# Optimization experiments

Measured on AMD Instinct MI355X. Metric: run time of the kernel, lower is better.

The kernel has to match this reference:

```python
import jax, jax.numpy as jnp
import numpy as np

N = 300000   # total nodes
C = 32       # hidden states
M = 64       # discrete label alphabet
NGEN = 8     # number of generative models
G = 8192     # number of graphs


def setup_inputs() -> dict:
    key = jax.random.key(0)
    k1, k2, k3, k4 = jax.random.split(key, 4)
    B = jax.random.uniform(k1, (C, M, NGEN), minval=-5.0, maxval=5.0, dtype=jnp.float32)
    Pi = jax.random.uniform(k2, (C, NGEN), minval=-5.0, maxval=5.0, dtype=jnp.float32)
    x = jax.random.randint(k3, (N,), 0, M)
    batch = jnp.sort(jax.random.randint(k4, (N,), 0, G))
    return {"B": B, "Pi": Pi, "x": x, "batch": batch, "num_graphs": G}


def reference(B, Pi, x, batch, num_graphs):
    # softmax reparameterization: over M for B, over C for Pi (per generator)
    sm_B = jax.nn.softmax(B, axis=1)          # (C, M, n_gen)
    sm_Pi = jax.nn.softmax(Pi, axis=0)        # (C, n_gen)
    # gather per-node emission probs, then joint with prior -> (N, C, n_gen)
    numerator = sm_Pi[None, :, :] * jnp.transpose(sm_B[:, x, :], (1, 0, 2))
    posterior = numerator / numerator.sum(axis=1, keepdims=True)  # (N, C, n_gen)
    likelihood = (posterior * jnp.log(numerator)).sum(axis=1)     # (N, n_gen)
    # scatter-sum per graph
    likelihood = jax.ops.segment_sum(likelihood, batch, num_segments=num_graphs)  # (G, n_gen)
    h_vals = posterior.max(axis=1, keepdims=True)   # (N, 1, n_gen)
    h_idx = posterior.argmax(axis=1)                # (N, n_gen)
    return likelihood, h_vals, h_idx
```

## Files before the change

kernel.cpp:

```cpp
#include <hip/hip_runtime.h>

#define C_DIM 32
#define M_DIM 64
#define NG    8
#define TAB   (M_DIM * NG)
#define ST    9
#define SPB   1024
#define NPB   512

__global__ void __launch_bounds__(256)
cgmm_prep(const float* __restrict__ B, const float* __restrict__ Pi,
          const int* __restrict__ batch,
          float* __restrict__ tab, int* __restrict__ starts,
          int N, int G, int nsb) {
    const int tid = threadIdx.x;

    if ((int)blockIdx.x < nsb) {
        const int base = blockIdx.x * SPB;
        for (int i = tid; i < SPB; i += 256) {
            const int n = base + i;
            if (n >= N) break;
            const int bn = batch[n];
            if (n == 0) {
                for (int j = 0; j <= bn; ++j) starts[j] = 0;
            } else {
                const int bp = batch[n - 1];
                for (int j = bp + 1; j <= bn; ++j) starts[j] = n;
            }
            if (n == N - 1) {
                for (int j = bn + 1; j <= G; ++j) starts[j] = N;
            }
        }
        return;
    }

    __shared__ float Pis[C_DIM * NG];
    __shared__ float lsePi_s[NG];
    __shared__ float K_s[C_DIM * NG];

    Pis[tid] = Pi[tid];
    __syncthreads();

    if (tid < NG) {
        float mx = -1e30f;
        #pragma unroll
        for (int c = 0; c < C_DIM; ++c) mx = fmaxf(mx, Pis[c * NG + tid]);
        float s = 0.f;
        #pragma unroll
        for (int c = 0; c < C_DIM; ++c) s += expf(Pis[c * NG + tid] - mx);
        lsePi_s[tid] = logf(s) + mx;
    }
    __syncthreads();

    {
        const int g = tid & 7;
        const float* bp = B + (tid >> 3) * (M_DIM * NG) + g;
        float mx = -1e30f;
        #pragma unroll
        for (int m = 0; m < M_DIM; ++m) mx = fmaxf(mx, bp[m * NG]);
        float s = 0.f;
        #pragma unroll
        for (int m = 0; m < M_DIM; ++m) s += expf(bp[m * NG] - mx);
        K_s[tid] = Pis[tid] - (logf(s) + mx) - lsePi_s[g];
    }
    __syncthreads();

    {
        const int q = tid >> 3, g = tid & 7;
        #pragma unroll
        for (int h = 0; h < 2; ++h) {
            const int m = q + 32 * h;
            float L[C_DIM];
            float best = -1e30f; int bidx = 0;
            #pragma unroll
            for (int c = 0; c < C_DIM; ++c) {
                float v = B[c * (M_DIM * NG) + m * NG + g] + K_s[c * NG + g];
                L[c] = v;
                if (v > best) { best = v; bidx = c; }
            }
            float se = 0.f, la = 0.f;
            #pragma unroll
            for (int c = 0; c < C_DIM; ++c) {
                float e = expf(L[c] - best);
                se += e; la += e * L[c];
            }
            const int idx = m * NG + g;
            tab[idx]           = la / se;
            tab[TAB + idx]     = 1.f / se;
            tab[2 * TAB + idx] = (float)bidx;
        }
    }
}

__global__ void __launch_bounds__(256)
cgmm_write(const int* __restrict__ x, const int* __restrict__ starts,
           const float* __restrict__ tab,
           float* __restrict__ out_like, float* __restrict__ out_hv,
           float* __restrict__ out_hi, int N, int G, int nnb) {
    const int tid = threadIdx.x;

    if ((int)blockIdx.x < nnb) {
        __shared__ float hval_s[M_DIM * ST];
        __shared__ float hidx_s[M_DIM * ST];
        __shared__ int   xs_s[NPB];
        const int base = blockIdx.x * NPB;

        for (int i = tid; i < TAB; i += 256) {
            const int m = i >> 3, g = i & 7;
            hval_s[m * ST + g] = tab[TAB + i];
            hidx_s[m * ST + g] = tab[2 * TAB + i];
        }
        for (int i = tid; i < NPB; i += 256) {
            const int n = base + i;
            if (n < N) xs_s[i] = x[n];
        }
        __syncthreads();

        const int s = tid >> 3, g = tid & 7;
        #pragma unroll
        for (int k = 0; k < NPB / 32; ++k) {
            const int i = k * 32 + s;
            const int n = base + i;
            if (n >= N) break;
            const int xm = xs_s[i];
            out_hv[(size_t)n * NG + g] = hval_s[xm * ST + g];
            out_hi[(size_t)n * NG + g] = hidx_s[xm * ST + g];
        }
        return;
    }

    __shared__ float like_s[M_DIM * ST];
    for (int i = tid; i < TAB; i += 256)
        like_s[(i >> 3) * ST + (i & 7)] = tab[i];
    __syncthreads();

    const int j = ((int)blockIdx.x - nnb) * 4 + (tid >> 6);
    if (j >= G) return;
    const int start = starts[j];
    const int end   = starts[j + 1];

    const int slot = (tid >> 3) & 7;
    const int g    = tid & 7;

    float acc = 0.f;
    for (int n = start + slot; n < end; n += 8)
        acc += like_s[x[n] * ST + g];

    acc += __shfl_xor(acc, 8);
    acc += __shfl_xor(acc, 16);
    acc += __shfl_xor(acc, 32);
    if ((tid & 63) < NG) out_like[(size_t)j * NG + g] = acc;
}

extern "C" void kernel_launch(void* const* d_in, const int* in_sizes, int n_in,
                              void* d_out, int out_size, void* d_ws, size_t ws_size,
                              hipStream_t stream) {
    const float* B     = (const float*)d_in[0];
    const float* Pi    = (const float*)d_in[1];
    const int*   x     = (const int*)d_in[2];
    const int*   batch = (const int*)d_in[3];
    const int N = in_sizes[2];
    const int G = (out_size - 2 * N * NG) / NG;

    float* tab    = (float*)d_ws;
    int*   starts = (int*)((char*)d_ws + 8192);

    float* out_like = (float*)d_out;
    float* out_hv   = out_like + (size_t)G * NG;
    float* out_hi   = out_hv + (size_t)N * NG;

    const int nsb = (N + SPB - 1) / SPB;
    const int nnb = (N + NPB - 1) / NPB;
    const int nlb = (G + 3) / 4;

    cgmm_prep<<<nsb + 1, 256, 0, stream>>>(B, Pi, batch, tab, starts, N, G, nsb);
    cgmm_write<<<nnb + nlb, 256, 0, stream>>>(x, starts, tab, out_like,
                                              out_hv, out_hi, N, G, nnb);
}
```

Before: 21.78 us.

## Fuse per-node hv/hi writes into per-graph segment loop; stage B in LDS

Result: faster. 19.98 us (-8.2%).

```diff
diff --git a/kernel.cpp b/kernel.cpp
--- a/kernel.cpp
+++ b/kernel.cpp
@@ -5,10 +5,10 @@
 #define NG    8
 #define TAB   (M_DIM * NG)
 #define ST    9
-#define SPB   1024
-#define NPB   512
+#define BST   520
+#define SPB   2048
 
-__global__ void __launch_bounds__(256)
+__global__ void __launch_bounds__(512)
 cgmm_prep(const float* __restrict__ B, const float* __restrict__ Pi,
           const int* __restrict__ batch,
           float* __restrict__ tab, int* __restrict__ starts,
@@ -17,7 +17,7 @@
 
     if ((int)blockIdx.x < nsb) {
         const int base = blockIdx.x * SPB;
-        for (int i = tid; i < SPB; i += 256) {
+        for (int i = tid; i < SPB; i += 512) {
             const int n = base + i;
             if (n >= N) break;
             const int bn = batch[n];
@@ -34,11 +34,20 @@
         return;
     }
 
+    __shared__ float Bs[C_DIM * BST];
     __shared__ float Pis[C_DIM * NG];
     __shared__ float lsePi_s[NG];
     __shared__ float K_s[C_DIM * NG];
 
-    Pis[tid] = Pi[tid];
+    {
+        const float4* B4 = (const float4*)B;
+        float4* Bs4 = (float4*)Bs;
+        #pragma unroll
+        for (int i = tid; i < (C_DIM * M_DIM * NG) / 4; i += 512) {
+            Bs4[(i >> 7) * (BST / 4) + (i & 127)] = B4[i];
+        }
+        if (tid < C_DIM * NG / 4) ((float4*)Pis)[tid] = ((const float4*)Pi)[tid];
+    }
     __syncthreads();
 
     if (tid < NG) {
@@ -52,9 +61,9 @@
     }
     __syncthreads();
 
-    {
-        const int g = tid & 7;
-        const float* bp = B + (tid >> 3) * (M_DIM * NG) + g;
+    if (tid < C_DIM * NG) {
+        const int c = tid >> 3, g = tid & 7;
+        const float* bp = Bs + c * BST + g;
         float mx = -1e30f;
         #pragma unroll
         for (int m = 0; m < M_DIM; ++m) mx = fmaxf(mx, bp[m * NG]);
@@ -66,29 +75,24 @@
     __syncthreads();
 
     {
-        const int q = tid >> 3, g = tid & 7;
+        const int m = tid >> 3, g = tid & 7;
+        float L[C_DIM];
+        float best = -1e30f; int bidx = 0;
         #pragma unroll
-        for (int h = 0; h < 2; ++h) {
-            const int m = q + 32 * h;
-            float L[C_DIM];
-            float best = -1e30f; int bidx = 0;
-            #pragma unroll
-            for (int c = 0; c < C_DIM; ++c) {
-                float v = B[c * (M_DIM * NG) + m * NG + g] + K_s[c * NG + g];
-                L[c] = v;
-                if (v > best) { best = v; bidx = c; }
-            }
-            float se = 0.f, la = 0.f;
-            #pragma unroll
-            for (int c = 0; c < C_DIM; ++c) {
-                float e = expf(L[c] - best);
-                se += e; la += e * L[c];
-            }
-            const int idx = m * NG + g;
-            tab[idx]           = la / se;
-            tab[TAB + idx]     = 1.f / se;
-            tab[2 * TAB + idx] = (float)bidx;
+        for (int c = 0; c < C_DIM; ++c) {
+            float v = Bs[c * BST + m * NG + g] + K_s[c * NG + g];
+            L[c] = v;
+            if (v > best) { best = v; bidx = c; }
         }
+        float se = 0.f, la = 0.f;
+        #pragma unroll
+        for (int c = 0; c < C_DIM; ++c) {
+            float e = expf(L[c] - best);
+            se += e; la += e * L[c];
+        }
+        tab[tid]           = la / se;
+        tab[TAB + tid]     = 1.f / se;
+        tab[2 * TAB + tid] = (float)bidx;
     }
 }
 
@@ -96,45 +100,20 @@
 cgmm_write(const int* __restrict__ x, const int* __restrict__ starts,
            const float* __restrict__ tab,
            float* __restrict__ out_like, float* __restrict__ out_hv,
-           float* __restrict__ out_hi, int N, int G, int nnb) {
+           float* __restrict__ out_hi, int G) {
+    __shared__ float like_s[M_DIM * ST];
+    __shared__ float hval_s[M_DIM * ST];
+    __shared__ float hidx_s[M_DIM * ST];
     const int tid = threadIdx.x;
-
-    if ((int)blockIdx.x < nnb) {
-        __shared__ float hval_s[M_DIM * ST];
-        __shared__ float hidx_s[M_DIM * ST];
-        __shared__ int   xs_s[NPB];
-        const int base = blockIdx.x * NPB;
-
-        for (int i = tid; i < TAB; i += 256) {
-            const int m = i >> 3, g = i & 7;
-            hval_s[m * ST + g] = tab[TAB + i];
-            hidx_s[m * ST + g] = tab[2 * TAB + i];
-        }
-        for (int i = tid; i < NPB; i += 256) {
-            const int n = base + i;
-            if (n < N) xs_s[i] = x[n];
-        }
-        __syncthreads();
-
-        const int s = tid >> 3, g = tid & 7;
-        #pragma unroll
-        for (int k = 0; k < NPB / 32; ++k) {
-            const int i = k * 32 + s;
-            const int n = base + i;
-            if (n >= N) break;
-            const int xm = xs_s[i];
-            out_hv[(size_t)n * NG + g] = hval_s[xm * ST + g];
-            out_hi[(size_t)n * NG + g] = hidx_s[xm * ST + g];
-        }
-        return;
+    for (int i = tid; i < TAB; i += 256) {
+        const int p = (i >> 3) * ST + (i & 7);
+        like_s[p] = tab[i];
+        hval_s[p] = tab[TAB + i];
+        hidx_s[p] = tab[2 * TAB + i];
     }
-
-    __shared__ float like_s[M_DIM * ST];
-    for (int i = tid; i < TAB; i += 256)
-        like_s[(i >> 3) * ST + (i & 7)] = tab[i];
     __syncthreads();
 
-    const int j = ((int)blockIdx.x - nnb) * 4 + (tid >> 6);
+    const int j = blockIdx.x * 4 + (tid >> 6);
     if (j >= G) return;
     const int start = starts[j];
     const int end   = starts[j + 1];
@@ -143,9 +122,13 @@
     const int g    = tid & 7;
 
     float acc = 0.f;
-    for (int n = start + slot; n < end; n += 8)
-        acc += like_s[x[n] * ST + g];
-
+    for (int n = start + slot; n < end; n += 8) {
+        const int xm = x[n];
+        const int p  = xm * ST + g;
+        acc += like_s[p];
+        out_hv[(size_t)n * NG + g] = hval_s[p];
+        out_hi[(size_t)n * NG + g] = hidx_s[p];
+    }
     acc += __shfl_xor(acc, 8);
     acc += __shfl_xor(acc, 16);
     acc += __shfl_xor(acc, 32);
@@ -170,10 +153,8 @@
     float* out_hi   = out_hv + (size_t)N * NG;
 
     const int nsb = (N + SPB - 1) / SPB;
-    const int nnb = (N + NPB - 1) / NPB;
-    const int nlb = (G + 3) / 4;
 
-    cgmm_prep<<<nsb + 1, 256, 0, stream>>>(B, Pi, batch, tab, starts, N, G, nsb);
-    cgmm_write<<<nnb + nlb, 256, 0, stream>>>(x, starts, tab, out_like,
-                                              out_hv, out_hi, N, G, nnb);
+    cgmm_prep<<<nsb + 1, 512, 0, stream>>>(B, Pi, batch, tab, starts, N, G, nsb);
+    cgmm_write<<<(G + 3) / 4, 256, 0, stream>>>(x, starts, tab, out_like,
+                                                out_hv, out_hi, G);
 }
```
